# Performance work log

Measured on AMD Instinct MI355X. Metric: run time of the kernel, lower is better.

Reference implementation:

```python
import jax, jax.numpy as jnp
import numpy as np

N_QUBITS = 9
C64 = jnp.complex64

PZ = jnp.array([[1, 0], [0, -1]], dtype=C64)
PX = jnp.array([[0, 1], [1, 0]], dtype=C64)
PY = jnp.array([[0, -1j], [1j, 0]], dtype=C64)
CNOT = jnp.array([[1, 0, 0, 0], [0, 1, 0, 0], [0, 0, 0, 1], [0, 0, 1, 0]], dtype=C64).reshape(2, 2, 2, 2)


def _rx(t):
    c = jnp.cos(t / 2).astype(C64)
    s = jnp.sin(t / 2).astype(C64)
    return jnp.stack([jnp.stack([c, -1j * s]), jnp.stack([-1j * s, c])])


def _ry(t):
    c = jnp.cos(t / 2).astype(C64)
    s = jnp.sin(t / 2).astype(C64)
    return jnp.stack([jnp.stack([c, -s]), jnp.stack([s, c])])


def _ap1(state, g, q):
    # apply 2x2 gate g on qubit axis q of state with shape (2,)*n
    return jnp.moveaxis(jnp.tensordot(g, state, axes=((1,), (q,))), 0, q)


def _ap2(state, g, q1, q2):
    return jnp.moveaxis(jnp.tensordot(g, state, axes=((2, 3), (q1, q2))), (0, 1), (q1, q2))


def _simulate(x, w, n, Denc, D):
    state = jnp.zeros((2,) * n, dtype=C64).at[(0,) * n].set(1.0)
    idx = 0
    for j in range(n):
        state = _ap1(state, _rx(x[idx]), j)
        state = _ap1(state, _ry(x[idx + 1]), j)
        idx += 2
    for _ in range(Denc):
        for j in range(n):
            state = _ap2(state, CNOT, j, (j + 1) % n)
        for j in range(n):
            state = _ap1(state, _ry(x[idx]), j)
            idx += 1
    idx = 0
    for j in range(n):
        state = _ap1(state, _rx(w[idx]), j)
        state = _ap1(state, _ry(w[idx + 1]), j)
        idx += 2
    for _ in range(D):
        for j in range(n):
            state = _ap2(state, CNOT, j, (j + 1) % n)
        for j in range(n):
            state = _ap1(state, _ry(w[idx]), j)
            idx += 1
    return state


def _expZ0(state):
    return jnp.real(jnp.vdot(state, _ap1(state, PZ, 0)))


def _expvals(state, n, ngroups):
    # E[p, q] = <Pauli_p on qubit q>; observable i -> qubit i%n, pauli (i//n)%3 (Z,X,Y)
    E = jnp.stack([jnp.stack([jnp.real(jnp.vdot(state, _ap1(state, P, q))) for q in range(n)])
                   for P in (PZ, PX, PY)])
    return jnp.concatenate([E[g % 3] for g in range(ngroups)])


def _forward(inp, wq, wk, wv):
    B, S, d = inp.shape
    n = N_QUBITS
    Denc = d // n - 2
    D = wq.shape[0] // n - 2
    flat = jnp.swapaxes(inp, 0, 1).reshape(S * B, d)  # matches torch transpose(0,1).reshape
    qk_fn = jax.vmap(lambda x, w: _expZ0(_simulate(x, w, n, Denc, D)), in_axes=(0, None))
    v_fn = jax.vmap(lambda x: _expvals(_simulate(x, wv, n, Denc, D), n, Denc + 2))
    Q = qk_fn(flat, wq).reshape(S, B, 1).swapaxes(0, 1).astype(inp.dtype)  # (B,S,1)
    K = qk_fn(flat, wk).reshape(S, B, 1).swapaxes(0, 1).astype(inp.dtype)
    V = v_fn(flat).reshape(S, B, d).swapaxes(0, 1).astype(inp.dtype)       # (B,S,d)
    alpha = jnp.exp(-(Q[:, :, None, :] - K[:, None, :, :]) ** 2)  # (B,S,S,1)
    alpha = alpha / jnp.sum(alpha, axis=2, keepdims=True)
    return inp + jnp.sum(alpha * V[:, None, :, :], axis=2)


def setup_inputs() -> dict:
    key = jax.random.key(0)
    k1, k2, k3, k4 = jax.random.split(key, 4)
    B, S, n, Denc, D = 48, 96, 9, 4, 8
    d = n * (Denc + 2)          # 54
    wdim = n * (D + 2)          # 90
    pi4 = np.float32(np.pi / 4)
    return {
        "input": jax.random.normal(k1, (B, S, d), dtype=jnp.float32),
        "params_Q": pi4 * (2 * jax.random.normal(k2, (wdim,), dtype=jnp.float32) - 1),
        "params_K": pi4 * (2 * jax.random.normal(k3, (wdim,), dtype=jnp.float32) - 1),
        "params_V": pi4 * (2 * jax.random.normal(k4, (wdim,), dtype=jnp.float32) - 1),
    }


def reference(input, params_Q, params_K, params_V):
    return _forward(input, params_Q, params_K, params_V)
```

## Files before the change

kernel.cpp:

```cpp
#include <hip/hip_runtime.h>
#include <math.h>

#define B_DIM  48
#define S_DIM  96
#define D_DIM  54
#define DENC   4
#define DVAR   8
#define NFLAT  (B_DIM * S_DIM)

typedef _Float16 h2 __attribute__((ext_vector_type(2)));

__device__ __forceinline__ int h2i(h2 v) { return __builtin_bit_cast(int, v); }
__device__ __forceinline__ h2  i2h(int v) { return __builtin_bit_cast(h2, v); }

__device__ __forceinline__ int pk_mul(int a, int b) {
    int d;
    asm("v_pk_mul_f16 %0, %1, %2" : "=v"(d) : "v"(a), "v"(b));
    return d;
}
__device__ __forceinline__ int pk_fma(int a, int b, int c) {
    int d;
    asm("v_pk_fma_f16 %0, %1, %2, %3" : "=v"(d) : "v"(a), "v"(b), "v"(c));
    return d;
}

template<int LM>
__device__ __forceinline__ int lxi(int x, int lane) {
    if constexpr (LM == 1)       return __builtin_amdgcn_update_dpp(x, x, 0xB1, 0xF, 0xF, true);
    else if constexpr (LM == 2)  return __builtin_amdgcn_update_dpp(x, x, 0x4E, 0xF, 0xF, true);
    else if constexpr (LM == 4)  return __builtin_amdgcn_ds_swizzle(x, 0x101F);
    else if constexpr (LM == 8)  return __builtin_amdgcn_update_dpp(x, x, 0x128, 0xF, 0xF, true);
    else if constexpr (LM == 16) return __builtin_amdgcn_ds_swizzle(x, 0x401F);
    else {
        auto r = __builtin_amdgcn_permlane32_swap(x, x, false, false);
        return (lane & 32) ? r[0] : r[1];
    }
}
template<int LM>
__device__ __forceinline__ float lx(float v, int lane) {
    return __int_as_float(lxi<LM>(__float_as_int(v), lane));
}

__device__ __forceinline__ float wave_sum(float v, int lane) {
    v += lx<32>(v, lane);
    v += lx<16>(v, lane);
    v += lx<8>(v, lane);
    v += lx<4>(v, lane);
    v += lx<2>(v, lane);
    v += lx<1>(v, lane);
    return v;
}


__device__ __forceinline__ int hswapi(int p) {
    return __builtin_amdgcn_alignbit(p, p, 16);
}

__device__ __forceinline__ void ring(h2 st[8], int lane) {
    const int gray = (lane ^ (lane >> 1)) << 2;
#pragma unroll
    for (int r = 0; r < 8; ++r)
        st[r] = i2h(__builtin_amdgcn_ds_bpermute(gray, h2i(st[r])));
    {
        const bool c0 = (lane & 1) != 0;
#pragma unroll
        for (int r = 0; r < 4; ++r) {
            h2 a = st[r], b = st[r + 4];
            st[r]     = c0 ? b : a;
            st[r + 4] = c0 ? a : b;
        }
    }
    { h2 t = st[4]; st[4] = st[6]; st[6] = t; }
    { h2 t = st[5]; st[5] = st[7]; st[7] = t; }
    { h2 t = st[2]; st[2] = st[3]; st[3] = t; }
    { h2 t = st[6]; st[6] = st[7]; st[7] = t; }
#pragma unroll
    for (int r = 1; r < 8; r += 2)
        st[r] = i2h(lxi<32>(h2i(st[r]), lane));
}

template<int BJ>
__device__ __forceinline__ void rot_ry(h2 st[8], int c2i, int s2i, int lane) {
    if constexpr (BJ >= 3) {
        constexpr int lm = 1 << (BJ - 3);
        const int sg = (lane & lm) ? s2i : (s2i ^ 0x80008000);
#pragma unroll
        for (int r = 0; r < 8; ++r) {
            int p = lxi<lm>(h2i(st[r]), lane);
            st[r] = i2h(pk_fma(p, sg, pk_mul(h2i(st[r]), c2i)));
        }
    } else {
        constexpr int M = 1 << BJ;
        const int ns2 = s2i ^ 0x80008000;
#pragma unroll
        for (int r = 0; r < 8; ++r) {
            if ((r & M) == 0) {
                int a = h2i(st[r]), b = h2i(st[r + M]);
                st[r]     = i2h(pk_fma(b, ns2, pk_mul(a, c2i)));
                st[r + M] = i2h(pk_fma(a, s2i, pk_mul(b, c2i)));
            }
        }
    }
}

template<int BJ>
__device__ __forceinline__ void rot_rx(h2 st[8], int c2i, int s2i, int lane) {
    const int sm = s2i ^ 0x80000000;
    if constexpr (BJ >= 3) {
        constexpr int lm = 1 << (BJ - 3);
#pragma unroll
        for (int r = 0; r < 8; ++r) {
            int p = lxi<lm>(h2i(st[r]), lane);
            st[r] = i2h(pk_fma(hswapi(p), sm, pk_mul(h2i(st[r]), c2i)));
        }
    } else {
        constexpr int M = 1 << BJ;
#pragma unroll
        for (int r = 0; r < 8; ++r) {
            if ((r & M) == 0) {
                int a = h2i(st[r]), b = h2i(st[r + M]);
                st[r]     = i2h(pk_fma(hswapi(b), sm, pk_mul(a, c2i)));
                st[r + M] = i2h(pk_fma(hswapi(a), sm, pk_mul(b, c2i)));
            }
        }
    }
}

#define INITQ(j) { rot_rx<8 - (j)>(st, cc[2 * (j)],     ss[2 * (j)],     lane);  \
                   rot_ry<8 - (j)>(st, cc[2 * (j) + 1], ss[2 * (j) + 1], lane); }

__device__ __forceinline__ void run_circuit(h2 st[8], const int* cc, const int* ss,
                                            int layers, int lane) {
    INITQ(0) INITQ(1) INITQ(2) INITQ(3) INITQ(4)
    INITQ(5) INITQ(6) INITQ(7) INITQ(8)
    const int* pc = cc + 18;
    const int* ps = ss + 18;
#pragma unroll 1
    for (int L = 0; L < layers; ++L) {
        ring(st, lane);
        rot_ry<8>(st, pc[0], ps[0], lane);
        rot_ry<7>(st, pc[1], ps[1], lane);
        rot_ry<6>(st, pc[2], ps[2], lane);
        rot_ry<5>(st, pc[3], ps[3], lane);
        rot_ry<4>(st, pc[4], ps[4], lane);
        rot_ry<3>(st, pc[5], ps[5], lane);
        rot_ry<2>(st, pc[6], ps[6], lane);
        rot_ry<1>(st, pc[7], ps[7], lane);
        rot_ry<0>(st, pc[8], ps[8], lane);
        pc += 9; ps += 9;
    }
}

template<int BJ>
__device__ __forceinline__ void expv(const h2 st[8], int lane, float& ez, float& ex, float& ey) {
    ez = ex = ey = 0.f;
    if constexpr (BJ >= 3) {
        constexpr int lm = 1 << (BJ - 3);
        const float sgn = (lane & lm) ? -1.f : 1.f;
#pragma unroll
        for (int r = 0; r < 8; ++r) {
            h2 p = i2h(lxi<lm>(h2i(st[r]), lane));
            float x = (float)st[r].x, y = (float)st[r].y;
            float px = (float)p.x,   py = (float)p.y;
            ez += sgn * (x * x + y * y);
            ex += x * px + y * py;
            ey += sgn * (x * py - y * px);
        }
    } else {
        constexpr int M = 1 << BJ;
#pragma unroll
        for (int r = 0; r < 8; ++r) {
            if ((r & M) == 0) {
                float ax = (float)st[r].x,     ay = (float)st[r].y;
                float bx = (float)st[r + M].x, by = (float)st[r + M].y;
                ez += (ax * ax + ay * ay) - (bx * bx + by * by);
                ex += 2.f * (ax * bx + ay * by);
                ey += 2.f * (ax * by - ay * bx);
            }
        }
    }
    ez = wave_sum(ez, lane); ex = wave_sum(ex, lane); ey = wave_sum(ey, lane);
}

__global__ __launch_bounds__(64) void sim_kernel(
    const float* __restrict__ inp, const float* __restrict__ wq,
    const float* __restrict__ wk,  const float* __restrict__ wv,
    float* __restrict__ outQ, float* __restrict__ outK, float* __restrict__ outV)
{
    __shared__ int csc[324];
    __shared__ int css[324];

    const int lane = threadIdx.x;
    const int fi   = blockIdx.x;
    const int b = fi % B_DIM, s = fi / B_DIM;
    const float* x = inp + ((size_t)b * S_DIM + s) * D_DIM;

    for (int k = lane; k < 324; k += 64) {
        float ang = (k < 54)  ? x[k]
                  : (k < 144) ? wq[k - 54]
                  : (k < 234) ? wk[k - 144]
                              : wv[k - 234];
        float sn, cn; sincosf(0.5f * ang, &sn, &cn);
        _Float16 hc = (_Float16)cn, hs = (_Float16)sn;
        h2 c2 = {hc, hc}, s2 = {hs, hs};
        csc[k] = h2i(c2);
        css[k] = h2i(s2);
    }

    h2 st[8], ck[8];
#pragma unroll
    for (int r = 0; r < 8; ++r) st[r] = i2h(0);
    if (lane == 0) { h2 one = {(_Float16)1.f, (_Float16)0.f}; st[0] = one; }

    run_circuit(st, csc, css, DENC, lane);
#pragma unroll
    for (int r = 0; r < 8; ++r) ck[r] = st[r];

    run_circuit(st, csc + 54, css + 54, DVAR, lane);
    {
        float p = 0.f;
#pragma unroll
        for (int r = 0; r < 8; ++r) {
            float xx = (float)st[r].x, yy = (float)st[r].y;
            p += xx * xx + yy * yy;
        }
        p = (lane & 32) ? -p : p;
        p = wave_sum(p, lane);
        if (lane == 0) outQ[fi] = p;
    }

#pragma unroll
    for (int r = 0; r < 8; ++r) st[r] = ck[r];
    run_circuit(st, csc + 144, css + 144, DVAR, lane);
    {
        float p = 0.f;
#pragma unroll
        for (int r = 0; r < 8; ++r) {
            float xx = (float)st[r].x, yy = (float)st[r].y;
            p += xx * xx + yy * yy;
        }
        p = (lane & 32) ? -p : p;
        p = wave_sum(p, lane);
        if (lane == 0) outK[fi] = p;
    }

#pragma unroll
    for (int r = 0; r < 8; ++r) st[r] = ck[r];
    run_circuit(st, csc + 234, css + 234, DVAR, lane);
    {
        float* vrow = outV + (size_t)fi * D_DIM;
#define EXPQ(q) { float ez, ex, ey; expv<8 - (q)>(st, lane, ez, ex, ey);            \
                  if (lane == 0) { vrow[(q)] = ez; vrow[9 + (q)] = ex;              \
                                   vrow[18 + (q)] = ey; vrow[27 + (q)] = ez;        \
                                   vrow[36 + (q)] = ex; vrow[45 + (q)] = ey; } }
        EXPQ(0) EXPQ(1) EXPQ(2) EXPQ(3) EXPQ(4)
        EXPQ(5) EXPQ(6) EXPQ(7) EXPQ(8)
#undef EXPQ
    }
}

__global__ __launch_bounds__(256) void attn_kernel(
    const float* __restrict__ inp, const float* __restrict__ Q,
    const float* __restrict__ K,   const float* __restrict__ V,
    float* __restrict__ out)
{
    __shared__ float w4[4][S_DIM];
    const int warp = threadIdx.x >> 6;
    const int t    = threadIdx.x & 63;
    const int bi   = blockIdx.x * 4 + warp;
    const int b    = bi / S_DIM;
    const int i    = bi % S_DIM;
    float* w = w4[warp];

    const float q = Q[i * B_DIM + b];
    float e0, e1 = 0.f;
    {
        float d0 = q - K[t * B_DIM + b];
        e0 = expf(-d0 * d0);
        w[t] = e0;
        if (t < S_DIM - 64) {
            float d1 = q - K[(t + 64) * B_DIM + b];
            e1 = expf(-d1 * d1);
            w[t + 64] = e1;
        }
    }
    float ps = wave_sum(e0 + e1, t);
    const float inv = 1.f / ps;

    if (t < D_DIM) {
        float acc = 0.f;
        for (int j = 0; j < S_DIM; ++j)
            acc += w[j] * V[(size_t)(j * B_DIM + b) * D_DIM + t];
        size_t o = (size_t)bi * D_DIM + t;
        out[o] = inp[o] + acc * inv;
    }
}

extern "C" void kernel_launch(void* const* d_in, const int* in_sizes, int n_in,
                              void* d_out, int out_size, void* d_ws, size_t ws_size,
                              hipStream_t stream)
{
    (void)in_sizes; (void)n_in; (void)out_size; (void)ws_size;
    const float* inp = (const float*)d_in[0];
    const float* wq  = (const float*)d_in[1];
    const float* wk  = (const float*)d_in[2];
    const float* wv  = (const float*)d_in[3];
    float* outp = (float*)d_out;

    float* Qw = (float*)d_ws;
    float* Kw = Qw + NFLAT;
    float* Vw = Kw + NFLAT;

    sim_kernel<<<NFLAT, 64, 0, stream>>>(inp, wq, wk, wv, Qw, Kw, Vw);
    attn_kernel<<<NFLAT / 4, 256, 0, stream>>>(inp, Qw, Kw, Vw, outp);
}
```

Baseline: 108.9 us.

## Split Q/K/V circuit simulations across separate blocks for more parallelism

Launches three blocks per input row, one each for the Q, K and V circuits. Each block recomputes the shared encoding circuit instead of checkpointing it and reusing it sequentially. This triples the block count (4608 to 13824 single-wave blocks) to raise occupancy and shorten each block's critical path. The cost is redundant encoding-circuit work and redundant sincos/input loads in every block.

```diff
diff --git a/kernel.cpp b/kernel.cpp
--- a/kernel.cpp
+++ b/kernel.cpp
@@ -187,19 +187,19 @@
     const float* __restrict__ wk,  const float* __restrict__ wv,
     float* __restrict__ outQ, float* __restrict__ outK, float* __restrict__ outV)
 {
-    __shared__ int csc[324];
-    __shared__ int css[324];
+    __shared__ int csc[144];
+    __shared__ int css[144];
 
     const int lane = threadIdx.x;
-    const int fi   = blockIdx.x;
+    const int gbl  = blockIdx.x;
+    const int cid  = gbl % 3;
+    const int fi   = gbl / 3;
     const int b = fi % B_DIM, s = fi / B_DIM;
     const float* x = inp + ((size_t)b * S_DIM + s) * D_DIM;
-
-    for (int k = lane; k < 324; k += 64) {
-        float ang = (k < 54)  ? x[k]
-                  : (k < 144) ? wq[k - 54]
-                  : (k < 234) ? wk[k - 144]
-                              : wv[k - 234];
+    const float* w = (cid == 0) ? wq : (cid == 1) ? wk : wv;
+
+    for (int k = lane; k < 144; k += 64) {
+        float ang = (k < 54) ? x[k] : w[k - 54];
         float sn, cn; sincosf(0.5f * ang, &sn, &cn);
         _Float16 hc = (_Float16)cn, hs = (_Float16)sn;
         h2 c2 = {hc, hc}, s2 = {hs, hs};
@@ -207,17 +207,15 @@
         css[k] = h2i(s2);
     }
 
-    h2 st[8], ck[8];
+    h2 st[8];
 #pragma unroll
     for (int r = 0; r < 8; ++r) st[r] = i2h(0);
     if (lane == 0) { h2 one = {(_Float16)1.f, (_Float16)0.f}; st[0] = one; }
 
     run_circuit(st, csc, css, DENC, lane);
-#pragma unroll
-    for (int r = 0; r < 8; ++r) ck[r] = st[r];
-
     run_circuit(st, csc + 54, css + 54, DVAR, lane);
-    {
+
+    if (cid < 2) {
         float p = 0.f;
 #pragma unroll
         for (int r = 0; r < 8; ++r) {
@@ -226,28 +224,8 @@
         }
         p = (lane & 32) ? -p : p;
         p = wave_sum(p, lane);
-        if (lane == 0) outQ[fi] = p;
-    }
-
-#pragma unroll
-    for (int r = 0; r < 8; ++r) st[r] = ck[r];
-    run_circuit(st, csc + 144, css + 144, DVAR, lane);
-    {
-        float p = 0.f;
-#pragma unroll
-        for (int r = 0; r < 8; ++r) {
-            float xx = (float)st[r].x, yy = (float)st[r].y;
-            p += xx * xx + yy * yy;
-        }
-        p = (lane & 32) ? -p : p;
-        p = wave_sum(p, lane);
-        if (lane == 0) outK[fi] = p;
-    }
-
-#pragma unroll
-    for (int r = 0; r < 8; ++r) st[r] = ck[r];
-    run_circuit(st, csc + 234, css + 234, DVAR, lane);
-    {
+        if (lane == 0) { if (cid == 0) outQ[fi] = p; else outK[fi] = p; }
+    } else {
         float* vrow = outV + (size_t)fi * D_DIM;
 #define EXPQ(q) { float ez, ex, ey; expv<8 - (q)>(st, lane, ez, ex, ey);            \
                   if (lane == 0) { vrow[(q)] = ez; vrow[9 + (q)] = ex;              \
@@ -311,6 +289,6 @@
     float* Kw = Qw + NFLAT;
     float* Vw = Kw + NFLAT;
 
-    sim_kernel<<<NFLAT, 64, 0, stream>>>(inp, wq, wk, wv, Qw, Kw, Vw);
+    sim_kernel<<<NFLAT * 3, 64, 0, stream>>>(inp, wq, wk, wv, Qw, Kw, Vw);
     attn_kernel<<<NFLAT / 4, 256, 0, stream>>>(inp, Qw, Kw, Vw, outp);
 }
```

Measured after the change: 119.1 us. 9.4% more time.
